# Optimization experiments

Hardware: AMD Instinct MI355X
Metric: run time of the kernel (lower is better)

The kernel has to match this reference:

```python
import jax, jax.numpy as jnp
import numpy as np

T_STEPS, B, I, H = 512, 64, 128, 256
LAST_K, RSIZE = 16, 32


def _xavier(key, shape):
    fan_out, fan_in = shape[0], shape[-1]
    std = (2.0 / (fan_in + fan_out)) ** 0.5
    return (std * jax.random.normal(key, shape)).astype(jnp.float32)


def setup_inputs() -> dict:
    key = jax.random.key(0)
    ks = jax.random.split(key, 8)
    inp = {"x": jax.random.normal(ks[0], (T_STEPS, B, I), dtype=jnp.float32)}
    for n, k in zip(["Wf", "Wi", "Wo", "Wg"], ks[1:5]):
        inp[n + "_w"] = _xavier(k, (H, H + I))
        inp[n + "_b"] = jnp.zeros((H,), jnp.float32)
    inp["Ua_w"] = _xavier(ks[5], (H, H))
    inp["Va_w"] = _xavier(ks[6], (H, H))
    inp["v"] = _xavier(ks[7], (1, H))
    return inp


def _forward(x, Wf_w, Wf_b, Wi_w, Wi_b, Wo_w, Wo_b, Wg_w, Wg_b, Ua_w, Va_w, v):
    T = x.shape[0]
    vv = v[0]  # [H]
    neg_inf = jnp.float32(-jnp.inf)

    def lstm(st, ct, xt):
        inp = jnp.concatenate([st, xt], axis=1)  # [B, H+I], order (hidden, input) as in torch cat((st, x), 1)
        ft = jax.nn.sigmoid(inp @ Wf_w.T + Wf_b)
        it = jax.nn.sigmoid(inp @ Wi_w.T + Wi_b)
        ot = jax.nn.sigmoid(inp @ Wo_w.T + Wo_b)
        gt = jnp.tanh(inp @ Wg_w.T + Wg_b)
        ct = ft * ct + it * gt
        return ot * jnp.tanh(ct), ct

    # ---- step 0 (reset path): st = zero hidden, no attention ----
    st0 = jnp.zeros((B, H), jnp.float32)
    h0, ct0 = lstm(st0, jnp.zeros((B, H), jnp.float32), x[0])
    mem0 = jnp.zeros((LAST_K, B, H), jnp.float32).at[-1].set(h0)  # ring of last_k hiddens (zeros = not yet filled)
    carry0 = (st0, ct0, mem0,
              jnp.zeros((RSIZE, B, H), jnp.float32),   # long_mem buckets
              jnp.full((RSIZE, B), neg_inf),            # long_mask (-inf = empty bucket)
              jnp.zeros((T, B), jnp.float32),           # long_scores (detached accumulator)
              jnp.zeros((B, RSIZE), jnp.float32),       # buck_scores
              jnp.zeros((B,), jnp.int32))               # per-sample bucket fill count

    def body(carry, tx):
        st, ct, mem, long_mem, long_mask, long_scores, buck, fill = carry
        t, xt = tx
        slots = jnp.arange(LAST_K)
        short_valid = slots >= (LAST_K - t)  # slot j holds h_{t-LAST_K+j}; valid iff time >= 0
        # ---- additive attention over short memory + long-term buckets ----
        q = st @ Va_w.T                              # [B,H]
        Uahs = mem @ Ua_w.T                          # [LAST_K,B,H]
        long_uas = long_mem @ Ua_w.T                 # [RSIZE,B,H]
        es = jnp.einsum('kbh,h->kb', jnp.tanh(q[None] + Uahs), vv)
        es = jnp.where(short_valid[:, None], es, neg_inf)
        es_long = jnp.einsum('rbh,h->rb', jnp.tanh(q[None] + long_uas), vv) + long_mask
        alphas = jax.nn.softmax(jnp.concatenate([es, es_long], 0), axis=0)  # [LAST_K+RSIZE,B]
        # accumulate detached attention mass onto absolute-time scores
        det_a = jax.lax.stop_gradient(alphas[:LAST_K])
        times = jnp.clip(t - LAST_K + slots, 0, T - 1)
        long_scores = long_scores.at[times].add(jnp.where(short_valid[:, None], det_a, 0.0))
        comb = jnp.concatenate([mem, long_mem], 0)   # [LAST_K+RSIZE,B,H]
        ct_att = jnp.einsum('nb,nbh->bh', alphas, comb)
        st = 0.5 * (mem[-1] + ct_att)                # comb_hs[-1-rsize] == previous hidden
        # ---- LSTM gating ----
        hidden, ct = lstm(st, ct, xt)
        # ---- bucket insert / argmin-replace (active once t >= LAST_K) ----
        cand = mem[0]                                # h_{t-LAST_K} == memory[0]
        cand_score = jax.lax.stop_gradient(
            jax.lax.dynamic_index_in_dim(long_scores, jnp.clip(t - LAST_K, 0, T - 1), 0, keepdims=False))  # [B]
        minp = jnp.argmin(buck, axis=1)              # [B], first-min like torch.argmin
        min_val = jnp.take_along_axis(buck, minp[:, None], axis=1)[:, 0]
        full = fill >= RSIZE
        addpos = jnp.where(full, minp, fill)
        do_upd = (t >= LAST_K) & (jnp.logical_not(full) | (cand_score > min_val))
        onehot = (jnp.arange(RSIZE)[None, :] == addpos[:, None]) & do_upd[:, None]  # [B,RSIZE]
        sel = onehot.T                               # [RSIZE,B]
        long_mem = jnp.where(sel[:, :, None], cand[None], long_mem)
        long_mask = jnp.where(sel, 0.0, long_mask)
        buck = jnp.where(onehot, cand_score[:, None], buck)
        fill = fill + (do_upd & jnp.logical_not(full)).astype(jnp.int32)
        # ---- push hidden into short-memory ring ----
        mem = jnp.concatenate([mem[1:], hidden[None]], 0)
        return (st, ct, mem, long_mem, long_mask, long_scores, buck, fill), hidden

    ts = jnp.arange(1, T)
    _, hs = jax.lax.scan(jax.checkpoint(body), carry0, (ts, x[1:]))
    return jnp.concatenate([h0[None], hs], 0)  # [T,B,H]


def reference(x, Wf_w, Wf_b, Wi_w, Wi_b, Wo_w, Wo_b, Wg_w, Wg_b, Ua_w, Va_w, v):
    return _forward(x, Wf_w, Wf_b, Wi_w, Wi_b, Wo_w, Wo_b, Wg_w, Wg_b, Ua_w, Va_w, v)
```

## Files before the change

kernel.cpp:

```cpp
#include <hip/hip_runtime.h>
#include <hip/hip_fp16.h>

#define T_STEPS 512
#define NB      64
#define NI      128
#define NH      256
#define LK      16
#define RS      32
#define NS      (LK + RS)

#define WP_OFF   0
#define VAP8_OFF 786432
#define UAP8_OFF 917504
#define LRAW_OFF 1048576
#define LUA_OFF  3145728
#define GX_OFF   5242880
#define WS_NEED  (GX_OFF + (size_t)T_STEPS * NB * NH * 8)

typedef _Float16 half2v __attribute__((ext_vector_type(2)));

__device__ __forceinline__ float hdot(unsigned int w, unsigned int s, float c) {
    return __builtin_amdgcn_fdot2(__builtin_bit_cast(half2v, w),
                                  __builtin_bit_cast(half2v, s), c, false);
}

__device__ __forceinline__ float fsig(float x) {
    return __builtin_amdgcn_rcpf(1.0f + __expf(-x));
}
__device__ __forceinline__ float ftanh(float x) {
    x = fminf(15.0f, fmaxf(-15.0f, x));
    float e = __expf(2.0f * x);
    return (e - 1.0f) * __builtin_amdgcn_rcpf(e + 1.0f);
}

__global__ void prep_weights(const float* __restrict__ Wf, const float* __restrict__ Wi,
                             const float* __restrict__ Wo, const float* __restrict__ Wg,
                             const float* __restrict__ Ua, const float* __restrict__ Va,
                             unsigned char* __restrict__ ws) {
    int e = blockIdx.x * 256 + threadIdx.x;
    if (e < 49152) {
        int h = e & 255, k2 = e >> 8, k = 2 * k2;
        uint4 w; __half2 t;
        t = __floats2half2_rn(Wf[h * 384 + k], Wf[h * 384 + k + 1]); w.x = *(unsigned int*)&t;
        t = __floats2half2_rn(Wi[h * 384 + k], Wi[h * 384 + k + 1]); w.y = *(unsigned int*)&t;
        t = __floats2half2_rn(Wo[h * 384 + k], Wo[h * 384 + k + 1]); w.z = *(unsigned int*)&t;
        t = __floats2half2_rn(Wg[h * 384 + k], Wg[h * 384 + k + 1]); w.w = *(unsigned int*)&t;
        ((uint4*)(ws + WP_OFF))[e] = w;
    } else {
        int e2 = e - 49152;
        const float* S = (e2 < 8192) ? Va : Ua;
        int e3 = e2 & 8191;
        int h = e3 & 255, j = e3 >> 8, k = 8 * j;
        uint4 w; __half2 t;
        t = __floats2half2_rn(S[h * 256 + k + 0], S[h * 256 + k + 1]); w.x = *(unsigned int*)&t;
        t = __floats2half2_rn(S[h * 256 + k + 2], S[h * 256 + k + 3]); w.y = *(unsigned int*)&t;
        t = __floats2half2_rn(S[h * 256 + k + 4], S[h * 256 + k + 5]); w.z = *(unsigned int*)&t;
        t = __floats2half2_rn(S[h * 256 + k + 6], S[h * 256 + k + 7]); w.w = *(unsigned int*)&t;
        ((uint4*)(ws + VAP8_OFF))[e2] = w;
    }
}

__global__ __launch_bounds__(256) void gx_gemm(const float* __restrict__ x,
                                               unsigned char* __restrict__ ws) {
    const int t = blockIdx.x, bg = blockIdx.y, tid = threadIdx.x;
    const uint4* __restrict__ WP = (const uint4*)(ws + WP_OFF);
    uint2* __restrict__ GX = (uint2*)(ws + GX_OFF);
    __shared__ float s_xx[16 * 128];
    const float* xb = x + ((size_t)t * NB + bg * 16) * NI;
#pragma unroll
    for (int r = 0; r < 8; ++r) s_xx[tid + 256 * r] = xb[tid + 256 * r];
    __syncthreads();
    const int h = tid;
    float acc[16][4];
#pragma unroll
    for (int bb = 0; bb < 16; ++bb) { acc[bb][0] = acc[bb][1] = acc[bb][2] = acc[bb][3] = 0.f; }
    for (int k2 = 128; k2 < 192; ++k2) {
        uint4 w = WP[k2 * NH + h];
        float2 wf = __half22float2(*(const __half2*)&w.x);
        float2 wi = __half22float2(*(const __half2*)&w.y);
        float2 wo = __half22float2(*(const __half2*)&w.z);
        float2 wg = __half22float2(*(const __half2*)&w.w);
        int kk = 2 * k2 - 256;
#pragma unroll
        for (int bb = 0; bb < 16; ++bb) {
            float2 xv = *(const float2*)(s_xx + bb * 128 + kk);
            acc[bb][0] += wf.x * xv.x + wf.y * xv.y;
            acc[bb][1] += wi.x * xv.x + wi.y * xv.y;
            acc[bb][2] += wo.x * xv.x + wo.y * xv.y;
            acc[bb][3] += wg.x * xv.x + wg.y * xv.y;
        }
    }
#pragma unroll
    for (int bb = 0; bb < 16; ++bb) {
        __half2 p0 = __floats2half2_rn(acc[bb][0], acc[bb][1]);
        __half2 p1 = __floats2half2_rn(acc[bb][2], acc[bb][3]);
        uint2 u; u.x = *(unsigned int*)&p0; u.y = *(unsigned int*)&p1;
        GX[((size_t)t * NB + bg * 16 + bb) * NH + h] = u;
    }
}

template <int USE_GX>
__global__ __launch_bounds__(1024, 1) void rel_lstm(
    const float* __restrict__ x,
    const float* __restrict__ bf_g, const float* __restrict__ bi_g,
    const float* __restrict__ bo_g, const float* __restrict__ bg_g,
    const float* __restrict__ vv_g,
    unsigned char* __restrict__ ws, float* __restrict__ out) {
    const int tid = threadIdx.x;
    const int b   = blockIdx.x;
    const int wv  = tid >> 6;
    const int ln  = tid & 63;
    const int h16 = (wv << 4) | (ln & 15);
    const int kc  = ln >> 4;

    const uint4* __restrict__ WP   = (const uint4*)(ws + WP_OFF);
    const uint4* __restrict__ VaP8 = (const uint4*)(ws + VAP8_OFF);
    const uint4* __restrict__ UaP8 = (const uint4*)(ws + UAP8_OFF);
    const uint2* __restrict__ GX   = (const uint2*)(ws + GX_OFF);
    float* __restrict__ lraw = (float*)(ws + LRAW_OFF) + b * (RS * NH);
    float* __restrict__ lua  = (float*)(ws + LUA_OFF)  + b * (RS * NH);

    __shared__ __align__(16) _Float16 s_in_h[NH + NI];
    __shared__ __align__(16) _Float16 s_hid_h[NH];
    __shared__ __align__(16) float s_q[NH];
    __shared__ __align__(16) float s_v[NH];
    __shared__ __align__(16) float s_mem[LK][NH];
    __shared__ __align__(16) float s_memua[LK][NH + 8];
    __shared__ float s_es[NS], s_al[NS];
    __shared__ float s_scores[T_STEPS];
    __shared__ float s_mask[RS], s_buck[RS];
    __shared__ float s_minv;
    __shared__ int s_minp, s_fill, s_upd, s_pos;

    for (int i = tid; i < LK * NH; i += 1024) ((float*)s_mem)[i] = 0.f;
    for (int i = tid; i < LK * (NH + 8); i += 1024) ((float*)s_memua)[i] = 0.f;
    if (tid < T_STEPS) s_scores[tid] = 0.f;
    if (tid < NH) s_v[tid] = vv_g[tid];
    if (tid < (NH + NI) / 2) ((unsigned int*)s_in_h)[tid] = 0u;
    if (tid < RS) { s_mask[tid] = -1e30f; s_buck[tid] = 0.f; }
    if (tid == 0) { s_fill = 0; s_upd = 0; s_pos = 0; s_minv = 0.f; s_minp = 0; }
    float bfv = 0.f, biv = 0.f, bov = 0.f, bgv = 0.f;
    if (kc == 0) { bfv = bf_g[h16]; biv = bi_g[h16]; bov = bo_g[h16]; bgv = bg_g[h16]; }
    if (!USE_GX && tid < 64) {
        float2 xv = ((const float2*)(x + (size_t)b * NI))[tid];
        __half2 hx = __floats2half2_rn(xv.x, xv.y);
        ((unsigned int*)s_in_h)[NH / 2 + tid] = *(unsigned int*)&hx;
    }
    float ct = 0.f;
    int base = 0;
    __syncthreads();

    for (int t = 0; t < T_STEPS; ++t) {
        float evA = 0.f, evB = 0.f;
        if (t > 0) {
            {
                const uint4* P   = (wv < 8) ? VaP8 : UaP8;
                const uint4* SRC = (wv < 8) ? (const uint4*)s_in_h : (const uint4*)s_hid_h;
                const int hh = ((wv & 7) << 5) | (ln & 31);
                const int ch = ln >> 5;
                float acc = 0.f;
#pragma unroll 8
                for (int jj = 0; jj < 16; ++jj) {
                    int j = (ch << 4) | jj;
                    uint4 w = P[(j << 8) + hh];
                    uint4 s = SRC[j];
                    acc = hdot(w.x, s.x, acc);
                    acc = hdot(w.y, s.y, acc);
                    acc = hdot(w.z, s.z, acc);
                    acc = hdot(w.w, s.w, acc);
                }
                acc += __shfl_xor(acc, 32, 64);
                if (ch == 0) {
                    if (wv < 8) s_q[hh] = acc;
                    else        s_memua[(base + LK - 1) & (LK - 1)][hh] = acc;
                }
                if (!USE_GX && tid < 64) {
                    float2 xv = ((const float2*)(x + ((size_t)t * NB + b) * NI))[tid];
                    __half2 hx = __floats2half2_rn(xv.x, xv.y);
                    ((unsigned int*)s_in_h)[NH / 2 + tid] = *(unsigned int*)&hx;
                }
            }
            __syncthreads();
            if (tid < 768) {
                const int row = tid >> 4, l = tid & 15;
                bool skip;
                const float* ua;
                if (row < LK) { skip = row < LK - t; ua = s_memua[(base + row) & (LK - 1)]; }
                else          { skip = s_mask[row - LK] < -1e29f; ua = lua + (row - LK) * NH; }
                float esv = -1e30f;
                if (!skip) {
                    float p = 0.f;
#pragma unroll
                    for (int jj = 0; jj < 4; ++jj) {
                        int hh = (l << 2) + (jj << 6);
                        float4 q4 = *(const float4*)(s_q + hh);
                        float4 v4 = *(const float4*)(s_v + hh);
                        float4 u4 = *(const float4*)(ua + hh);
                        p += v4.x * ftanh(q4.x + u4.x);
                        p += v4.y * ftanh(q4.y + u4.y);
                        p += v4.z * ftanh(q4.z + u4.z);
                        p += v4.w * ftanh(q4.w + u4.w);
                    }
                    p += __shfl_xor(p, 1, 16);
                    p += __shfl_xor(p, 2, 16);
                    p += __shfl_xor(p, 4, 16);
                    p += __shfl_xor(p, 8, 16);
                    esv = p;
                }
                if (l == 0) s_es[row] = esv;
            } else if (tid >= 960 && tid < 992) {
                int l = tid - 960;
                float v = s_buck[l]; int idx = l;
#pragma unroll
                for (int off = 1; off < 32; off <<= 1) {
                    float v2 = __shfl_xor(v, off, 32);
                    int  i2 = __shfl_xor(idx, off, 32);
                    if (v2 < v || (v2 == v && i2 < idx)) { v = v2; idx = i2; }
                }
                if (l == 0) { s_minv = v; s_minp = idx; }
            }
            __syncthreads();
            if (tid < 64) {
                float e = (tid < NS) ? s_es[tid] : -1e30f;
                float m = e;
#pragma unroll
                for (int off = 32; off; off >>= 1) m = fmaxf(m, __shfl_xor(m, off, 64));
                float a = (tid < NS) ? __expf(e - m) : 0.f;
                float ssum = a;
#pragma unroll
                for (int off = 32; off; off >>= 1) ssum += __shfl_xor(ssum, off, 64);
                float al = a * __builtin_amdgcn_rcpf(ssum);
                if (tid < NS) s_al[tid] = al;
                float cs = 0.f;
                if (tid < LK) {
                    int time = t - LK + tid;
                    if (time >= 0) {
                        float ns = s_scores[time] + al;
                        s_scores[time] = ns;
                        cs = ns;
                    }
                }
                if (tid == 0) {
                    int upd = 0, pos = 0;
                    if (t >= LK) {
                        int fill = s_fill;
                        bool full = fill >= RS;
                        upd = (!full) || (cs > s_minv);
                        pos = full ? s_minp : fill;
                        if (upd) { s_mask[pos] = 0.f; s_buck[pos] = cs; if (!full) s_fill = fill + 1; }
                    }
                    s_upd = upd; s_pos = pos;
                }
            }
            __syncthreads();
            {
                float catt = 0.f;
                const int n0 = kc * 12;
#pragma unroll
                for (int n = n0; n < n0 + 12; ++n) {
                    float a = s_al[n];
                    if (n < LK) catt += a * s_mem[(base + n) & (LK - 1)][h16];
                    else if (a != 0.f) catt += a * lraw[(n - LK) * NH + h16];
                }
                catt += __shfl_xor(catt, 16, 64);
                catt += __shfl_xor(catt, 32, 64);
                if (kc == 1 && s_upd) {
                    int p0 = base & (LK - 1);
                    evA = s_mem[p0][h16];
                    evB = s_memua[p0][h16];
                }
                if (kc == 0) {
                    float stv = 0.5f * (s_mem[(base + LK - 1) & (LK - 1)][h16] + catt);
                    s_in_h[h16] = (_Float16)stv;
                }
            }
            __syncthreads();
        }
        {
            uint2 gx = {0u, 0u};
            if (USE_GX && kc == 0) gx = GX[((size_t)t * NB + b) * NH + h16];
            constexpr int KP = USE_GX ? 32 : 48;
            const unsigned int* S2 = (const unsigned int*)s_in_h;
            float af = 0.f, ai = 0.f, ao = 0.f, ag = 0.f;
            const int lo = kc * KP;
#pragma unroll 8
            for (int k2 = lo; k2 < lo + KP; ++k2) {
                uint4 w = WP[(k2 << 8) + h16];
                unsigned int s2 = S2[k2];
                af = hdot(w.x, s2, af);
                ai = hdot(w.y, s2, ai);
                ao = hdot(w.z, s2, ao);
                ag = hdot(w.w, s2, ag);
            }
            af += __shfl_xor(af, 16, 64); af += __shfl_xor(af, 32, 64);
            ai += __shfl_xor(ai, 16, 64); ai += __shfl_xor(ai, 32, 64);
            ao += __shfl_xor(ao, 16, 64); ao += __shfl_xor(ao, 32, 64);
            ag += __shfl_xor(ag, 16, 64); ag += __shfl_xor(ag, 32, 64);
            if (kc == 0) {
                float pf = af + bfv, pi = ai + biv, po = ao + bov, pg = ag + bgv;
                if (USE_GX) {
                    float2 fi = __half22float2(*(const __half2*)&gx.x);
                    float2 og = __half22float2(*(const __half2*)&gx.y);
                    pf += fi.x; pi += fi.y; po += og.x; pg += og.y;
                }
                float f  = fsig(pf);
                float ii = fsig(pi);
                float o  = fsig(po);
                float g  = ftanh(pg);
                ct = f * ct + ii * g;
                float hid = o * ftanh(ct);
                out[((size_t)t * NB + b) * NH + h16] = hid;
                s_mem[base & (LK - 1)][h16] = hid;
                s_hid_h[h16] = (_Float16)hid;
            } else if (kc == 1 && s_upd) {
                lraw[s_pos * NH + h16] = evA;
                lua[s_pos * NH + h16]  = evB;
            }
        }
        base++;
        __syncthreads();
    }
}

extern "C" void kernel_launch(void* const* d_in, const int* in_sizes, int n_in,
                              void* d_out, int out_size, void* d_ws, size_t ws_size,
                              hipStream_t stream) {
    const float* x  = (const float*)d_in[0];
    const float* Wf = (const float*)d_in[1];
    const float* bf = (const float*)d_in[2];
    const float* Wi = (const float*)d_in[3];
    const float* bi = (const float*)d_in[4];
    const float* Wo = (const float*)d_in[5];
    const float* bo = (const float*)d_in[6];
    const float* Wg = (const float*)d_in[7];
    const float* bg = (const float*)d_in[8];
    const float* Ua = (const float*)d_in[9];
    const float* Va = (const float*)d_in[10];
    const float* vv = (const float*)d_in[11];
    unsigned char* ws = (unsigned char*)d_ws;
    float* out = (float*)d_out;

    prep_weights<<<256, 256, 0, stream>>>(Wf, Wi, Wo, Wg, Ua, Va, ws);
    if (ws_size >= WS_NEED) {
        gx_gemm<<<dim3(T_STEPS, 4), 256, 0, stream>>>(x, ws);
        rel_lstm<1><<<NB, 1024, 0, stream>>>(x, bf, bi, bo, bg, vv, ws, out);
    } else {
        rel_lstm<0><<<NB, 1024, 0, stream>>>(x, bf, bi, bo, bg, vv, ws, out);
    }
}
```

Measured before the change: 5.917 ms.

## Keep long-memory buckets in LDS and attention weights in registers

```diff
diff --git a/kernel.cpp b/kernel.cpp
--- a/kernel.cpp
+++ b/kernel.cpp
@@ -117,8 +117,6 @@
     const uint4* __restrict__ VaP8 = (const uint4*)(ws + VAP8_OFF);
     const uint4* __restrict__ UaP8 = (const uint4*)(ws + UAP8_OFF);
     const uint2* __restrict__ GX   = (const uint2*)(ws + GX_OFF);
-    float* __restrict__ lraw = (float*)(ws + LRAW_OFF) + b * (RS * NH);
-    float* __restrict__ lua  = (float*)(ws + LUA_OFF)  + b * (RS * NH);
 
     __shared__ __align__(16) _Float16 s_in_h[NH + NI];
     __shared__ __align__(16) _Float16 s_hid_h[NH];
@@ -126,14 +124,27 @@
     __shared__ __align__(16) float s_v[NH];
     __shared__ __align__(16) float s_mem[LK][NH];
     __shared__ __align__(16) float s_memua[LK][NH + 8];
+    __shared__ __align__(16) float s_lraw[RS * NH];
+    __shared__ __align__(16) float s_lua[RS * NH];
     __shared__ float s_es[NS], s_al[NS];
     __shared__ float s_scores[T_STEPS];
     __shared__ float s_mask[RS], s_buck[RS];
     __shared__ float s_minv;
     __shared__ int s_minp, s_fill, s_upd, s_pos;
 
+    const int p1_hh = ((wv & 7) << 5) | (ln & 31);
+    const int p1_ch = ln >> 5;
+    uint4 wreg[16];
+    {
+        const uint4* P = (wv < 8) ? VaP8 : UaP8;
+#pragma unroll
+        for (int jj = 0; jj < 16; ++jj)
+            wreg[jj] = P[(((p1_ch << 4) | jj) << 8) + p1_hh];
+    }
+
     for (int i = tid; i < LK * NH; i += 1024) ((float*)s_mem)[i] = 0.f;
     for (int i = tid; i < LK * (NH + 8); i += 1024) ((float*)s_memua)[i] = 0.f;
+    for (int i = tid; i < RS * NH; i += 1024) { s_lraw[i] = 0.f; s_lua[i] = 0.f; }
     if (tid < T_STEPS) s_scores[tid] = 0.f;
     if (tid < NH) s_v[tid] = vv_g[tid];
     if (tid < (NH + NI) / 2) ((unsigned int*)s_in_h)[tid] = 0u;
@@ -152,27 +163,29 @@
 
     for (int t = 0; t < T_STEPS; ++t) {
         float evA = 0.f, evB = 0.f;
+        uint2 gx = {0u, 0u};
+        if (USE_GX && kc == 0) gx = GX[((size_t)t * NB + b) * NH + h16];
         if (t > 0) {
             {
-                const uint4* P   = (wv < 8) ? VaP8 : UaP8;
                 const uint4* SRC = (wv < 8) ? (const uint4*)s_in_h : (const uint4*)s_hid_h;
-                const int hh = ((wv & 7) << 5) | (ln & 31);
-                const int ch = ln >> 5;
                 float acc = 0.f;
-#pragma unroll 8
+#pragma unroll
                 for (int jj = 0; jj < 16; ++jj) {
-                    int j = (ch << 4) | jj;
-                    uint4 w = P[(j << 8) + hh];
-                    uint4 s = SRC[j];
-                    acc = hdot(w.x, s.x, acc);
-                    acc = hdot(w.y, s.y, acc);
-                    acc = hdot(w.z, s.z, acc);
-                    acc = hdot(w.w, s.w, acc);
+                    uint4 s = SRC[(p1_ch << 4) | jj];
+                    acc = hdot(wreg[jj].x, s.x, acc);
+                    acc = hdot(wreg[jj].y, s.y, acc);
+                    acc = hdot(wreg[jj].z, s.z, acc);
+                    acc = hdot(wreg[jj].w, s.w, acc);
                 }
                 acc += __shfl_xor(acc, 32, 64);
-                if (ch == 0) {
-                    if (wv < 8) s_q[hh] = acc;
-                    else        s_memua[(base + LK - 1) & (LK - 1)][hh] = acc;
+                if (p1_ch == 0) {
+                    if (wv < 8) s_q[p1_hh] = acc;
+                    else        s_memua[(base + LK - 1) & (LK - 1)][p1_hh] = acc;
+                }
+                if (kc == 1) {
+                    int p0 = base & (LK - 1);
+                    evA = s_mem[p0][h16];
+                    evB = s_memua[p0][h16];
                 }
                 if (!USE_GX && tid < 64) {
                     float2 xv = ((const float2*)(x + ((size_t)t * NB + b) * NI))[tid];
@@ -186,7 +199,7 @@
                 bool skip;
                 const float* ua;
                 if (row < LK) { skip = row < LK - t; ua = s_memua[(base + row) & (LK - 1)]; }
-                else          { skip = s_mask[row - LK] < -1e29f; ua = lua + (row - LK) * NH; }
+                else          { skip = s_mask[row - LK] < -1e29f; ua = s_lua + (row - LK) * NH; }
                 float esv = -1e30f;
                 if (!skip) {
                     float p = 0.f;
@@ -260,15 +273,10 @@
                 for (int n = n0; n < n0 + 12; ++n) {
                     float a = s_al[n];
                     if (n < LK) catt += a * s_mem[(base + n) & (LK - 1)][h16];
-                    else if (a != 0.f) catt += a * lraw[(n - LK) * NH + h16];
+                    else if (a != 0.f) catt += a * s_lraw[(n - LK) * NH + h16];
                 }
                 catt += __shfl_xor(catt, 16, 64);
                 catt += __shfl_xor(catt, 32, 64);
-                if (kc == 1 && s_upd) {
-                    int p0 = base & (LK - 1);
-                    evA = s_mem[p0][h16];
-                    evB = s_memua[p0][h16];
-                }
                 if (kc == 0) {
                     float stv = 0.5f * (s_mem[(base + LK - 1) & (LK - 1)][h16] + catt);
                     s_in_h[h16] = (_Float16)stv;
@@ -277,8 +285,6 @@
             __syncthreads();
         }
         {
-            uint2 gx = {0u, 0u};
-            if (USE_GX && kc == 0) gx = GX[((size_t)t * NB + b) * NH + h16];
             constexpr int KP = USE_GX ? 32 : 48;
             const unsigned int* S2 = (const unsigned int*)s_in_h;
             float af = 0.f, ai = 0.f, ao = 0.f, ag = 0.f;
@@ -313,8 +319,8 @@
                 s_mem[base & (LK - 1)][h16] = hid;
                 s_hid_h[h16] = (_Float16)hid;
             } else if (kc == 1 && s_upd) {
-                lraw[s_pos * NH + h16] = evA;
-                lua[s_pos * NH + h16]  = evB;
+                s_lraw[s_pos * NH + h16] = evA;
+                s_lua[s_pos * NH + h16]  = evB;
             }
         }
         base++;
```

Measured after the change: 5.757 ms. 2.7% less time.

## Pack two batch samples per block and keep long-memory buckets in LDS as fp16

Applied to the files above, without the earlier changes.

```diff
diff --git a/kernel.cpp b/kernel.cpp
--- a/kernel.cpp
+++ b/kernel.cpp
@@ -12,8 +12,6 @@
 #define WP_OFF   0
 #define VAP8_OFF 786432
 #define UAP8_OFF 917504
-#define LRAW_OFF 1048576
-#define LUA_OFF  3145728
 #define GX_OFF   5242880
 #define WS_NEED  (GX_OFF + (size_t)T_STEPS * NB * NH * 8)
 
@@ -99,8 +97,215 @@
     }
 }
 
+__global__ __launch_bounds__(1024, 1) void rel_lstm2(
+    const float* __restrict__ bf_g, const float* __restrict__ bi_g,
+    const float* __restrict__ bo_g, const float* __restrict__ bg_g,
+    const float* __restrict__ vv_g,
+    unsigned char* __restrict__ ws, float* __restrict__ out) {
+    const int tid  = threadIdx.x;
+    const int wv   = tid >> 6, ln = tid & 63;
+    const int smp  = wv >> 3;
+    const int swv  = wv & 7;
+    const int stid = (swv << 6) | ln;
+    const int b    = blockIdx.x * 2 + smp;
+    const int p1_mat = stid >> 8;
+    const int p1_h   = stid & 255;
+    const int h32  = (swv << 5) | (ln & 31);
+    const int kc2  = ln >> 5;
+
+    const uint4* __restrict__ WP   = (const uint4*)(ws + WP_OFF);
+    const uint4* __restrict__ VaP8 = (const uint4*)(ws + VAP8_OFF);
+    const uint4* __restrict__ UaP8 = (const uint4*)(ws + UAP8_OFF);
+    const uint2* __restrict__ GX   = (const uint2*)(ws + GX_OFF);
+
+    __shared__ __align__(16) _Float16 s_in_h[2][NH];
+    __shared__ __align__(16) _Float16 s_hid_h[2][NH];
+    __shared__ __align__(16) float s_q[2][NH];
+    __shared__ __align__(16) float s_v[NH];
+    __shared__ __align__(16) float s_mem[2][LK][NH];
+    __shared__ __align__(16) float s_memua[2][LK][NH + 8];
+    __shared__ __align__(16) _Float16 s_lraw[2][RS][NH + 8];
+    __shared__ __align__(16) _Float16 s_lua[2][RS][NH + 8];
+    __shared__ float s_es[2][NS];
+    __shared__ float s_scores[2][T_STEPS];
+    __shared__ float s_buck[2][RS];
+    __shared__ float s_minv[2];
+    __shared__ int s_minp[2], s_fill[2], s_upd[2], s_pos[2];
+
+    for (int i = tid; i < 2 * LK * NH; i += 1024) ((float*)s_mem)[i] = 0.f;
+    for (int i = tid; i < 2 * LK * (NH + 8); i += 1024) ((float*)s_memua)[i] = 0.f;
+    for (int i = tid; i < 2 * RS * (NH + 8); i += 1024) {
+        ((_Float16*)s_lraw)[i] = (_Float16)0.f; ((_Float16*)s_lua)[i] = (_Float16)0.f;
+    }
+    ((float*)s_scores)[tid] = 0.f;
+    if (tid < NH) s_v[tid] = vv_g[tid];
+    if (tid < 2 * NH) { ((_Float16*)s_in_h)[tid] = (_Float16)0.f; ((_Float16*)s_hid_h)[tid] = (_Float16)0.f; }
+    if (tid < 2 * RS) ((float*)s_buck)[tid] = 0.f;
+    if (tid < 2) { s_fill[tid] = 0; s_upd[tid] = 0; s_pos[tid] = 0; s_minv[tid] = 0.f; s_minp[tid] = 0; }
+    float bfv = 0.f, biv = 0.f, bov = 0.f, bgv = 0.f;
+    if (kc2 == 0) { bfv = bf_g[h32]; biv = bi_g[h32]; bov = bo_g[h32]; bgv = bg_g[h32]; }
+    float ct = 0.f;
+    int base = 0;
+    __syncthreads();
+
+    for (int t = 0; t < T_STEPS; ++t) {
+        float evA = 0.f, evB = 0.f;
+        uint2 gx = {0u, 0u};
+        if (kc2 == 0) gx = GX[((size_t)t * NB + b) * NH + h32];
+        if (t > 0) {
+            {
+                const uint4* P   = p1_mat ? UaP8 : VaP8;
+                const uint4* SRC = p1_mat ? (const uint4*)s_hid_h[smp] : (const uint4*)s_in_h[smp];
+                float acc = 0.f;
+#pragma unroll 8
+                for (int j = 0; j < 32; ++j) {
+                    uint4 w = P[(j << 8) + p1_h];
+                    uint4 s = SRC[j];
+                    acc = hdot(w.x, s.x, acc);
+                    acc = hdot(w.y, s.y, acc);
+                    acc = hdot(w.z, s.z, acc);
+                    acc = hdot(w.w, s.w, acc);
+                }
+                if (p1_mat) {
+                    s_memua[smp][(base + LK - 1) & (LK - 1)][p1_h] = acc;
+                } else {
+                    s_q[smp][p1_h] = acc;
+                    evA = s_mem[smp][base & (LK - 1)][p1_h];
+                    evB = s_memua[smp][base & (LK - 1)][p1_h];
+                }
+            }
+            __syncthreads();
+            if (stid < 384) {
+                const int row = stid >> 3, l3 = stid & 7;
+                bool skip;
+                const float* uaf = nullptr;
+                const _Float16* uah = nullptr;
+                if (row < LK) { skip = row < LK - t; uaf = s_memua[smp][(base + row) & (LK - 1)]; }
+                else          { skip = (row - LK) >= s_fill[smp]; uah = s_lua[smp][row - LK]; }
+                float esv = -1e30f;
+                if (!skip) {
+                    float p = 0.f;
+#pragma unroll
+                    for (int jj = 0; jj < 8; ++jj) {
+                        int hh = (l3 << 2) + (jj << 5);
+                        float4 q4 = *(const float4*)(&s_q[smp][hh]);
+                        float4 v4 = *(const float4*)(&s_v[hh]);
+                        float4 u4;
+                        if (row < LK) {
+                            u4 = *(const float4*)(uaf + hh);
+                        } else {
+                            uint2 uh = *(const uint2*)(uah + hh);
+                            float2 a0 = __half22float2(*(const __half2*)&uh.x);
+                            float2 a1 = __half22float2(*(const __half2*)&uh.y);
+                            u4 = make_float4(a0.x, a0.y, a1.x, a1.y);
+                        }
+                        p += v4.x * ftanh(q4.x + u4.x);
+                        p += v4.y * ftanh(q4.y + u4.y);
+                        p += v4.z * ftanh(q4.z + u4.z);
+                        p += v4.w * ftanh(q4.w + u4.w);
+                    }
+                    p += __shfl_xor(p, 1, 8);
+                    p += __shfl_xor(p, 2, 8);
+                    p += __shfl_xor(p, 4, 8);
+                    esv = p;
+                }
+                if (l3 == 0) s_es[smp][row] = esv;
+            } else if (stid >= 448 && stid < 480) {
+                int l = stid - 448;
+                float v = s_buck[smp][l]; int idx = l;
+#pragma unroll
+                for (int off = 1; off < 32; off <<= 1) {
+                    float v2 = __shfl_xor(v, off, 32);
+                    int  i2 = __shfl_xor(idx, off, 32);
+                    if (v2 < v || (v2 == v && i2 < idx)) { v = v2; idx = i2; }
+                }
+                if (l == 0) { s_minv[smp] = v; s_minp[smp] = idx; }
+            }
+            __syncthreads();
+            {
+                float e = (ln < NS) ? s_es[smp][ln] : -1e30f;
+                float m = e;
+#pragma unroll
+                for (int off = 32; off; off >>= 1) m = fmaxf(m, __shfl_xor(m, off));
+                float a = (ln < NS) ? __expf(e - m) : 0.f;
+                float ssum = a;
+#pragma unroll
+                for (int off = 32; off; off >>= 1) ssum += __shfl_xor(ssum, off);
+                float al = a * __builtin_amdgcn_rcpf(ssum);
+                if (swv == 0) {
+                    float cs = 0.f;
+                    if (ln < LK) {
+                        int time = t - LK + ln;
+                        if (time >= 0) { float ns = s_scores[smp][time] + al; s_scores[smp][time] = ns; cs = ns; }
+                    }
+                    if (ln == 0) {
+                        int upd = 0, pos = 0;
+                        if (t >= LK) {
+                            int fill = s_fill[smp];
+                            bool full = fill >= RS;
+                            upd = (!full) || (cs > s_minv[smp]);
+                            pos = full ? s_minp[smp] : fill;
+                            if (upd) { s_buck[smp][pos] = cs; if (!full) s_fill[smp] = fill + 1; }
+                        }
+                        s_upd[smp] = upd; s_pos[smp] = pos;
+                    }
+                }
+                float catt = 0.f;
+#pragma unroll
+                for (int i = 0; i < 24; ++i) {
+                    int n = kc2 * 24 + i;
+                    float a2 = __shfl(al, n);
+                    if (n < LK) catt += a2 * s_mem[smp][(base + n) & (LK - 1)][h32];
+                    else if (a2 != 0.f) catt += a2 * (float)s_lraw[smp][n - LK][h32];
+                }
+                catt += __shfl_xor(catt, 32);
+                if (kc2 == 0) {
+                    float stv = 0.5f * (s_mem[smp][(base + LK - 1) & (LK - 1)][h32] + catt);
+                    s_in_h[smp][h32] = (_Float16)stv;
+                }
+            }
+            __syncthreads();
+        }
+        {
+            const unsigned int* S2 = (const unsigned int*)s_in_h[smp];
+            float af = 0.f, ai = 0.f, ao = 0.f, ag = 0.f;
+            const int lo = kc2 * 64;
+#pragma unroll 8
+            for (int k2 = lo; k2 < lo + 64; ++k2) {
+                uint4 w = WP[(k2 << 8) + h32];
+                unsigned int s2 = S2[k2];
+                af = hdot(w.x, s2, af);
+                ai = hdot(w.y, s2, ai);
+                ao = hdot(w.z, s2, ao);
+                ag = hdot(w.w, s2, ag);
+            }
+            af += __shfl_xor(af, 32); ai += __shfl_xor(ai, 32);
+            ao += __shfl_xor(ao, 32); ag += __shfl_xor(ag, 32);
+            if (kc2 == 0) {
+                float2 fi = __half22float2(*(const __half2*)&gx.x);
+                float2 og = __half22float2(*(const __half2*)&gx.y);
+                float f  = fsig(af + fi.x + bfv);
+                float ii = fsig(ai + fi.y + biv);
+                float o  = fsig(ao + og.x + bov);
+                float g  = ftanh(ag + og.y + bgv);
+                ct = f * ct + ii * g;
+                float hid = o * ftanh(ct);
+                out[((size_t)t * NB + b) * NH + h32] = hid;
+                s_mem[smp][base & (LK - 1)][h32] = hid;
+                s_hid_h[smp][h32] = (_Float16)hid;
+            }
+            if (p1_mat == 0 && s_upd[smp]) {
+                s_lraw[smp][s_pos[smp]][p1_h] = (_Float16)evA;
+                s_lua[smp][s_pos[smp]][p1_h]  = (_Float16)evB;
+            }
+        }
+        base++;
+        __syncthreads();
+    }
+}
+
 template <int USE_GX>
-__global__ __launch_bounds__(1024, 1) void rel_lstm(
+__global__ __launch_bounds__(1024, 1) void rel_lstm_mono(
     const float* __restrict__ x,
     const float* __restrict__ bf_g, const float* __restrict__ bi_g,
     const float* __restrict__ bo_g, const float* __restrict__ bg_g,
@@ -117,8 +322,6 @@
     const uint4* __restrict__ VaP8 = (const uint4*)(ws + VAP8_OFF);
     const uint4* __restrict__ UaP8 = (const uint4*)(ws + UAP8_OFF);
     const uint2* __restrict__ GX   = (const uint2*)(ws + GX_OFF);
-    float* __restrict__ lraw = (float*)(ws + LRAW_OFF) + b * (RS * NH);
-    float* __restrict__ lua  = (float*)(ws + LUA_OFF)  + b * (RS * NH);
 
     __shared__ __align__(16) _Float16 s_in_h[NH + NI];
     __shared__ __align__(16) _Float16 s_hid_h[NH];
@@ -126,6 +329,8 @@
     __shared__ __align__(16) float s_v[NH];
     __shared__ __align__(16) float s_mem[LK][NH];
     __shared__ __align__(16) float s_memua[LK][NH + 8];
+    __shared__ __align__(16) float s_lraw[RS * NH];
+    __shared__ __align__(16) float s_lua[RS * NH];
     __shared__ float s_es[NS], s_al[NS];
     __shared__ float s_scores[T_STEPS];
     __shared__ float s_mask[RS], s_buck[RS];
@@ -134,6 +339,7 @@
 
     for (int i = tid; i < LK * NH; i += 1024) ((float*)s_mem)[i] = 0.f;
     for (int i = tid; i < LK * (NH + 8); i += 1024) ((float*)s_memua)[i] = 0.f;
+    for (int i = tid; i < RS * NH; i += 1024) { s_lraw[i] = 0.f; s_lua[i] = 0.f; }
     if (tid < T_STEPS) s_scores[tid] = 0.f;
     if (tid < NH) s_v[tid] = vv_g[tid];
     if (tid < (NH + NI) / 2) ((unsigned int*)s_in_h)[tid] = 0u;
@@ -152,6 +358,8 @@
 
     for (int t = 0; t < T_STEPS; ++t) {
         float evA = 0.f, evB = 0.f;
+        uint2 gx = {0u, 0u};
+        if (USE_GX && kc == 0) gx = GX[((size_t)t * NB + b) * NH + h16];
         if (t > 0) {
             {
                 const uint4* P   = (wv < 8) ? VaP8 : UaP8;
@@ -159,7 +367,7 @@
                 const int hh = ((wv & 7) << 5) | (ln & 31);
                 const int ch = ln >> 5;
                 float acc = 0.f;
-#pragma unroll 8
+#pragma unroll
                 for (int jj = 0; jj < 16; ++jj) {
                     int j = (ch << 4) | jj;
                     uint4 w = P[(j << 8) + hh];
@@ -174,6 +382,11 @@
                     if (wv < 8) s_q[hh] = acc;
                     else        s_memua[(base + LK - 1) & (LK - 1)][hh] = acc;
                 }
+                if (kc == 1) {
+                    int p0 = base & (LK - 1);
+                    evA = s_mem[p0][h16];
+                    evB = s_memua[p0][h16];
+                }
                 if (!USE_GX && tid < 64) {
                     float2 xv = ((const float2*)(x + ((size_t)t * NB + b) * NI))[tid];
                     __half2 hx = __floats2half2_rn(xv.x, xv.y);
@@ -186,7 +399,7 @@
                 bool skip;
                 const float* ua;
                 if (row < LK) { skip = row < LK - t; ua = s_memua[(base + row) & (LK - 1)]; }
-                else          { skip = s_mask[row - LK] < -1e29f; ua = lua + (row - LK) * NH; }
+                else          { skip = s_mask[row - LK] < -1e29f; ua = s_lua + (row - LK) * NH; }
                 float esv = -1e30f;
                 if (!skip) {
                     float p = 0.f;
@@ -260,15 +473,10 @@
                 for (int n = n0; n < n0 + 12; ++n) {
                     float a = s_al[n];
                     if (n < LK) catt += a * s_mem[(base + n) & (LK - 1)][h16];
-                    else if (a != 0.f) catt += a * lraw[(n - LK) * NH + h16];
+                    else if (a != 0.f) catt += a * s_lraw[(n - LK) * NH + h16];
                 }
                 catt += __shfl_xor(catt, 16, 64);
                 catt += __shfl_xor(catt, 32, 64);
-                if (kc == 1 && s_upd) {
-                    int p0 = base & (LK - 1);
-                    evA = s_mem[p0][h16];
-                    evB = s_memua[p0][h16];
-                }
                 if (kc == 0) {
                     float stv = 0.5f * (s_mem[(base + LK - 1) & (LK - 1)][h16] + catt);
                     s_in_h[h16] = (_Float16)stv;
@@ -277,8 +485,6 @@
             __syncthreads();
         }
         {
-            uint2 gx = {0u, 0u};
-            if (USE_GX && kc == 0) gx = GX[((size_t)t * NB + b) * NH + h16];
             constexpr int KP = USE_GX ? 32 : 48;
             const unsigned int* S2 = (const unsigned int*)s_in_h;
             float af = 0.f, ai = 0.f, ao = 0.f, ag = 0.f;
@@ -313,8 +519,8 @@
                 s_mem[base & (LK - 1)][h16] = hid;
                 s_hid_h[h16] = (_Float16)hid;
             } else if (kc == 1 && s_upd) {
-                lraw[s_pos * NH + h16] = evA;
-                lua[s_pos * NH + h16]  = evB;
+                s_lraw[s_pos * NH + h16] = evA;
+                s_lua[s_pos * NH + h16]  = evB;
             }
         }
         base++;
@@ -343,8 +549,8 @@
     prep_weights<<<256, 256, 0, stream>>>(Wf, Wi, Wo, Wg, Ua, Va, ws);
     if (ws_size >= WS_NEED) {
         gx_gemm<<<dim3(T_STEPS, 4), 256, 0, stream>>>(x, ws);
-        rel_lstm<1><<<NB, 1024, 0, stream>>>(x, bf, bi, bo, bg, vv, ws, out);
+        rel_lstm2<<<NB / 2, 1024, 0, stream>>>(bf, bi, bo, bg, vv, ws, out);
     } else {
-        rel_lstm<0><<<NB, 1024, 0, stream>>>(x, bf, bi, bo, bg, vv, ws, out);
-    }
-}
+        rel_lstm_mono<0><<<NB, 1024, 0, stream>>>(x, bf, bi, bo, bg, vv, ws, out);
+    }
+}
```

After: 10.95 ms. +85.0%, slower.

## Keep long-memory buckets in LDS and prefetch LSTM weights across barriers

Applied to the files above, without the earlier changes.

```diff
diff --git a/kernel.cpp b/kernel.cpp
--- a/kernel.cpp
+++ b/kernel.cpp
@@ -12,8 +12,6 @@
 #define WP_OFF   0
 #define VAP8_OFF 786432
 #define UAP8_OFF 917504
-#define LRAW_OFF 1048576
-#define LUA_OFF  3145728
 #define GX_OFF   5242880
 #define WS_NEED  (GX_OFF + (size_t)T_STEPS * NB * NH * 8)
 
@@ -117,8 +115,6 @@
     const uint4* __restrict__ VaP8 = (const uint4*)(ws + VAP8_OFF);
     const uint4* __restrict__ UaP8 = (const uint4*)(ws + UAP8_OFF);
     const uint2* __restrict__ GX   = (const uint2*)(ws + GX_OFF);
-    float* __restrict__ lraw = (float*)(ws + LRAW_OFF) + b * (RS * NH);
-    float* __restrict__ lua  = (float*)(ws + LUA_OFF)  + b * (RS * NH);
 
     __shared__ __align__(16) _Float16 s_in_h[NH + NI];
     __shared__ __align__(16) _Float16 s_hid_h[NH];
@@ -126,6 +122,8 @@
     __shared__ __align__(16) float s_v[NH];
     __shared__ __align__(16) float s_mem[LK][NH];
     __shared__ __align__(16) float s_memua[LK][NH + 8];
+    __shared__ __align__(16) float s_lraw[RS * NH];
+    __shared__ __align__(16) float s_lua[RS * NH];
     __shared__ float s_es[NS], s_al[NS];
     __shared__ float s_scores[T_STEPS];
     __shared__ float s_mask[RS], s_buck[RS];
@@ -134,6 +132,7 @@
 
     for (int i = tid; i < LK * NH; i += 1024) ((float*)s_mem)[i] = 0.f;
     for (int i = tid; i < LK * (NH + 8); i += 1024) ((float*)s_memua)[i] = 0.f;
+    for (int i = tid; i < RS * NH; i += 1024) { s_lraw[i] = 0.f; s_lua[i] = 0.f; }
     if (tid < T_STEPS) s_scores[tid] = 0.f;
     if (tid < NH) s_v[tid] = vv_g[tid];
     if (tid < (NH + NI) / 2) ((unsigned int*)s_in_h)[tid] = 0u;
@@ -150,8 +149,13 @@
     int base = 0;
     __syncthreads();
 
+    constexpr int KP = USE_GX ? 32 : 48;
+    const int lo = kc * KP;
+
     for (int t = 0; t < T_STEPS; ++t) {
         float evA = 0.f, evB = 0.f;
+        uint2 gx = {0u, 0u};
+        if (USE_GX && kc == 0) gx = GX[((size_t)t * NB + b) * NH + h16];
         if (t > 0) {
             {
                 const uint4* P   = (wv < 8) ? VaP8 : UaP8;
@@ -159,7 +163,7 @@
                 const int hh = ((wv & 7) << 5) | (ln & 31);
                 const int ch = ln >> 5;
                 float acc = 0.f;
-#pragma unroll 8
+#pragma unroll
                 for (int jj = 0; jj < 16; ++jj) {
                     int j = (ch << 4) | jj;
                     uint4 w = P[(j << 8) + hh];
@@ -174,6 +178,11 @@
                     if (wv < 8) s_q[hh] = acc;
                     else        s_memua[(base + LK - 1) & (LK - 1)][hh] = acc;
                 }
+                if (kc == 1) {
+                    int p0 = base & (LK - 1);
+                    evA = s_mem[p0][h16];
+                    evB = s_memua[p0][h16];
+                }
                 if (!USE_GX && tid < 64) {
                     float2 xv = ((const float2*)(x + ((size_t)t * NB + b) * NI))[tid];
                     __half2 hx = __floats2half2_rn(xv.x, xv.y);
@@ -181,12 +190,22 @@
                 }
             }
             __syncthreads();
+        }
+        uint4 wA0 = WP[((lo + 0) << 8) + h16];
+        uint4 wA1 = WP[((lo + 1) << 8) + h16];
+        uint4 wA2 = WP[((lo + 2) << 8) + h16];
+        uint4 wA3 = WP[((lo + 3) << 8) + h16];
+        uint4 wA4 = WP[((lo + 4) << 8) + h16];
+        uint4 wA5 = WP[((lo + 5) << 8) + h16];
+        uint4 wA6 = WP[((lo + 6) << 8) + h16];
+        uint4 wA7 = WP[((lo + 7) << 8) + h16];
+        if (t > 0) {
             if (tid < 768) {
                 const int row = tid >> 4, l = tid & 15;
                 bool skip;
                 const float* ua;
                 if (row < LK) { skip = row < LK - t; ua = s_memua[(base + row) & (LK - 1)]; }
-                else          { skip = s_mask[row - LK] < -1e29f; ua = lua + (row - LK) * NH; }
+                else          { skip = s_mask[row - LK] < -1e29f; ua = s_lua + (row - LK) * NH; }
                 float esv = -1e30f;
                 if (!skip) {
                     float p = 0.f;
@@ -220,6 +239,16 @@
                 if (l == 0) { s_minv = v; s_minp = idx; }
             }
             __syncthreads();
+        }
+        uint4 wB0 = WP[((lo +  8) << 8) + h16];
+        uint4 wB1 = WP[((lo +  9) << 8) + h16];
+        uint4 wB2 = WP[((lo + 10) << 8) + h16];
+        uint4 wB3 = WP[((lo + 11) << 8) + h16];
+        uint4 wB4 = WP[((lo + 12) << 8) + h16];
+        uint4 wB5 = WP[((lo + 13) << 8) + h16];
+        uint4 wB6 = WP[((lo + 14) << 8) + h16];
+        uint4 wB7 = WP[((lo + 15) << 8) + h16];
+        if (t > 0) {
             if (tid < 64) {
                 float e = (tid < NS) ? s_es[tid] : -1e30f;
                 float m = e;
@@ -260,15 +289,10 @@
                 for (int n = n0; n < n0 + 12; ++n) {
                     float a = s_al[n];
                     if (n < LK) catt += a * s_mem[(base + n) & (LK - 1)][h16];
-                    else if (a != 0.f) catt += a * lraw[(n - LK) * NH + h16];
+                    else if (a != 0.f) catt += a * s_lraw[(n - LK) * NH + h16];
                 }
                 catt += __shfl_xor(catt, 16, 64);
                 catt += __shfl_xor(catt, 32, 64);
-                if (kc == 1 && s_upd) {
-                    int p0 = base & (LK - 1);
-                    evA = s_mem[p0][h16];
-                    evB = s_memua[p0][h16];
-                }
                 if (kc == 0) {
                     float stv = 0.5f * (s_mem[(base + LK - 1) & (LK - 1)][h16] + catt);
                     s_in_h[h16] = (_Float16)stv;
@@ -277,14 +301,32 @@
             __syncthreads();
         }
         {
-            uint2 gx = {0u, 0u};
-            if (USE_GX && kc == 0) gx = GX[((size_t)t * NB + b) * NH + h16];
-            constexpr int KP = USE_GX ? 32 : 48;
             const unsigned int* S2 = (const unsigned int*)s_in_h;
             float af = 0.f, ai = 0.f, ao = 0.f, ag = 0.f;
-            const int lo = kc * KP;
-#pragma unroll 8
-            for (int k2 = lo; k2 < lo + KP; ++k2) {
+            {
+                unsigned int s2;
+                s2 = S2[lo + 0]; af = hdot(wA0.x, s2, af); ai = hdot(wA0.y, s2, ai); ao = hdot(wA0.z, s2, ao); ag = hdot(wA0.w, s2, ag);
+                s2 = S2[lo + 1]; af = hdot(wA1.x, s2, af); ai = hdot(wA1.y, s2, ai); ao = hdot(wA1.z, s2, ao); ag = hdot(wA1.w, s2, ag);
+                s2 = S2[lo + 2]; af = hdot(wA2.x, s2, af); ai = hdot(wA2.y, s2, ai); ao = hdot(wA2.z, s2, ao); ag = hdot(wA2.w, s2, ag);
+                s2 = S2[lo + 3]; af = hdot(wA3.x, s2, af); ai = hdot(wA3.y, s2, ai); ao = hdot(wA3.z, s2, ao); ag = hdot(wA3.w, s2, ag);
+                s2 = S2[lo + 4]; af = hdot(wA4.x, s2, af); ai = hdot(wA4.y, s2, ai); ao = hdot(wA4.z, s2, ao); ag = hdot(wA4.w, s2, ag);
+                s2 = S2[lo + 5]; af = hdot(wA5.x, s2, af); ai = hdot(wA5.y, s2, ai); ao = hdot(wA5.z, s2, ao); ag = hdot(wA5.w, s2, ag);
+                s2 = S2[lo + 6]; af = hdot(wA6.x, s2, af); ai = hdot(wA6.y, s2, ai); ao = hdot(wA6.z, s2, ao); ag = hdot(wA6.w, s2, ag);
+                s2 = S2[lo + 7]; af = hdot(wA7.x, s2, af); ai = hdot(wA7.y, s2, ai); ao = hdot(wA7.z, s2, ao); ag = hdot(wA7.w, s2, ag);
+            }
+            {
+                unsigned int s2;
+                s2 = S2[lo +  8]; af = hdot(wB0.x, s2, af); ai = hdot(wB0.y, s2, ai); ao = hdot(wB0.z, s2, ao); ag = hdot(wB0.w, s2, ag);
+                s2 = S2[lo +  9]; af = hdot(wB1.x, s2, af); ai = hdot(wB1.y, s2, ai); ao = hdot(wB1.z, s2, ao); ag = hdot(wB1.w, s2, ag);
+                s2 = S2[lo + 10]; af = hdot(wB2.x, s2, af); ai = hdot(wB2.y, s2, ai); ao = hdot(wB2.z, s2, ao); ag = hdot(wB2.w, s2, ag);
+                s2 = S2[lo + 11]; af = hdot(wB3.x, s2, af); ai = hdot(wB3.y, s2, ai); ao = hdot(wB3.z, s2, ao); ag = hdot(wB3.w, s2, ag);
+                s2 = S2[lo + 12]; af = hdot(wB4.x, s2, af); ai = hdot(wB4.y, s2, ai); ao = hdot(wB4.z, s2, ao); ag = hdot(wB4.w, s2, ag);
+                s2 = S2[lo + 13]; af = hdot(wB5.x, s2, af); ai = hdot(wB5.y, s2, ai); ao = hdot(wB5.z, s2, ao); ag = hdot(wB5.w, s2, ag);
+                s2 = S2[lo + 14]; af = hdot(wB6.x, s2, af); ai = hdot(wB6.y, s2, ai); ao = hdot(wB6.z, s2, ao); ag = hdot(wB6.w, s2, ag);
+                s2 = S2[lo + 15]; af = hdot(wB7.x, s2, af); ai = hdot(wB7.y, s2, ai); ao = hdot(wB7.z, s2, ao); ag = hdot(wB7.w, s2, ag);
+            }
+#pragma unroll 2
+            for (int k2 = lo + 16; k2 < lo + KP; ++k2) {
                 uint4 w = WP[(k2 << 8) + h16];
                 unsigned int s2 = S2[k2];
                 af = hdot(w.x, s2, af);
@@ -313,8 +355,8 @@
                 s_mem[base & (LK - 1)][h16] = hid;
                 s_hid_h[h16] = (_Float16)hid;
             } else if (kc == 1 && s_upd) {
-                lraw[s_pos * NH + h16] = evA;
-                lua[s_pos * NH + h16]  = evB;
+                s_lraw[s_pos * NH + h16] = evA;
+                s_lua[s_pos * NH + h16]  = evB;
             }
         }
         base++;
```

New measurement: 6.927 ms. 17.1% more time.
